# Optimization experiments

Measured on AMD Instinct MI355X. Metric: run time of the kernel, lower is better.

Reference implementation:

```python
import jax, jax.numpy as jnp
import numpy as np

D_MODEL = 768
NUM_HEADS = 12
D_K = D_MODEL // NUM_HEADS


def setup_inputs() -> dict:
    key = jax.random.key(0)
    ks = jax.random.split(key, 9)
    B, N, C = 32, 577, D_MODEL
    s = 1.0 / np.sqrt(C)
    x = jax.random.normal(ks[0], (B, N, C), dtype=jnp.float32)
    Wq = jax.random.normal(ks[1], (C, C), dtype=jnp.float32) * s
    bq = jnp.zeros((C,), dtype=jnp.float32)
    Wk = jax.random.normal(ks[2], (C, C), dtype=jnp.float32) * s
    bk = jnp.zeros((C,), dtype=jnp.float32)
    Wv = jax.random.normal(ks[3], (C, C), dtype=jnp.float32) * s
    bv = jnp.zeros((C,), dtype=jnp.float32)
    Wo = jax.random.normal(ks[4], (C, C), dtype=jnp.float32) * s
    bo = jnp.zeros((C,), dtype=jnp.float32)
    return {"x": x, "Wq": Wq, "bq": bq, "Wk": Wk, "bk": bk,
            "Wv": Wv, "bv": bv, "Wo": Wo, "bo": bo}


def reference(x, Wq, bq, Wk, bk, Wv, bv, Wo, bo):
    B, N, C = x.shape
    H, dk = NUM_HEADS, D_K
    # Linear projections (torch Linear: x @ W.T + b)
    q = (x @ Wq.T + bq).reshape(B, N, H, dk).transpose(0, 2, 1, 3)  # [B,H,N,dk]
    k = (x @ Wk.T + bk).reshape(B, N, H, dk).transpose(0, 2, 1, 3)
    v = (x @ Wv.T + bv).reshape(B, N, H, dk).transpose(0, 2, 1, 3)
    scale = 1.0 / jnp.sqrt(jnp.asarray(dk, dtype=x.dtype))
    scores = jnp.einsum('bhnd,bhmd->bhnm', q, k) * scale  # [B,H,N,N]
    attn = jax.nn.softmax(scores, axis=-1)
    out = jnp.einsum('bhnm,bhmd->bhnd', attn, v)  # [B,H,N,dk]
    out = out.transpose(0, 2, 1, 3).reshape(B, N, C)
    return out @ Wo.T + bo
```

## Files before the change

kernel.cpp:

```cpp
#include <hip/hip_runtime.h>
#include <cstdint>
#include <cstddef>

typedef float  f32x4   __attribute__((ext_vector_type(4)));
typedef __bf16 bf16x8  __attribute__((ext_vector_type(8)));
typedef short  short8  __attribute__((ext_vector_type(8)));
typedef short  short4v __attribute__((ext_vector_type(4)));
typedef float  float4v __attribute__((ext_vector_type(4)));

#define DEVI __device__ __forceinline__

constexpr int Bb = 32, Nn = 577, Cc = 768, Hh = 12, DK = 64;
constexpr int Mm   = Bb * Nn;
constexpr int NQKV = 3 * Cc;
constexpr int NKPAD = 640;
constexpr int NT = 10;
#define QSCALE 0.1803368926f

DEVI short f2bf(float f) {
  __bf16 h = (__bf16)f;
  short s;
  __builtin_memcpy(&s, &h, 2);
  return s;
}

DEVI void gload16(const short* g, short* l) {
  __builtin_amdgcn_global_load_lds(
      (const __attribute__((address_space(1))) void*)g,
      (__attribute__((address_space(3))) void*)l, 16, 0, 0);
}

DEVI f32x4 mfma16(bf16x8 a, bf16x8 b, f32x4 c) {
  return __builtin_amdgcn_mfma_f32_16x16x32_bf16(a, b, c, 0, 0, 0);
}

DEVI void remap_grouped(int bid, int nbm, int nbn, int GM, int& bm, int& bn) {
  const int nwg = nbm * nbn;
  const int xcd = bid & 7, j = bid >> 3;
  const int q = nwg >> 3, r = nwg & 7;
  int wg = (xcd < r ? xcd * (q + 1) : r * (q + 1) + (xcd - r) * q) + j;
  const int per = GM * nbn;
  int grp = wg / per;
  int first = grp * GM;
  int sz = min(GM, nbm - first);
  int rem = wg - grp * per;
  bm = first + rem % sz;
  bn = rem / sz;
}


__global__ void k_cvt(const float* __restrict__ in, short* __restrict__ out, int n4) {
  int i = blockIdx.x * 256 + threadIdx.x;
  if (i >= n4) return;
  float4v v = *(const float4v*)(in + (size_t)i * 4);
  short4v o;
#pragma unroll
  for (int j = 0; j < 4; ++j) o[j] = f2bf(v[j]);
  *(short4v*)(out + (size_t)i * 4) = o;
}

__global__ void k_cvt_wqkv(const float* __restrict__ Wq, const float* __restrict__ Wk,
                           const float* __restrict__ Wv, short* __restrict__ out) {
  int i = blockIdx.x * 256 + threadIdx.x;
  int e = i * 4;
  if (e >= NQKV * Cc) return;
  const int WSZ = Cc * Cc;
  const float* src;
  if (e < WSZ)          src = Wq + e;
  else if (e < 2 * WSZ) src = Wk + (e - WSZ);
  else                  src = Wv + (e - 2 * WSZ);
  float4v v = *(const float4v*)src;
  short4v o;
#pragma unroll
  for (int j = 0; j < 4; ++j) o[j] = f2bf(v[j]);
  *(short4v*)(out + (size_t)e) = o;
}


#define WAITV(N) asm volatile("s_waitcnt vmcnt(" #N ")" ::: "memory")

#define PHASE(DKH, MH, STAGE_STMT, WAIT_STMT)                              \
  {                                                                        \
    const short* Ab_ = Al + (DKH) * 8192;                                  \
    const short* Bb_ = Bl + (DKH) * 8192;                                  \
    bf16x8 af_[4];                                                         \
    _Pragma("unroll")                                                      \
    for (int m_ = 0; m_ < 4; ++m_)                                         \
      af_[m_] = *(const bf16x8*)(Ab_ + offA[(MH) * 4 + m_]);               \
    if ((MH) == 0) {                                                       \
      _Pragma("unroll")                                                    \
      for (int n_ = 0; n_ < 4; ++n_)                                       \
        bfr[n_] = *(const bf16x8*)(Bb_ + offB[n_]);                        \
    }                                                                      \
    STAGE_STMT;                                                            \
    WAIT_STMT;                                                             \
    __builtin_amdgcn_s_barrier();                                          \
    __builtin_amdgcn_s_setprio(1);                                         \
    _Pragma("unroll")                                                      \
    for (int m_ = 0; m_ < 4; ++m_)                                         \
      _Pragma("unroll")                                                    \
      for (int n_ = 0; n_ < 4; ++n_)                                       \
        acc[(MH) * 4 + m_][n_] = mfma16(af_[m_], bfr[n_], acc[(MH) * 4 + m_][n_]); \
    __builtin_amdgcn_s_setprio(0);                                         \
    __builtin_amdgcn_s_barrier();                                          \
  }

DEVI void gemm256_core(const short* __restrict__ A, const short* __restrict__ Bm,
                       int arows, int bm, int bn,
                       short* Al, short* Bl, f32x4 acc[8][4]) {
  const int tid = threadIdx.x;
  const int lane = tid & 63, w = tid >> 6;
  const int wm = w >> 2, wn = w & 3;
  const int qi = lane & 15, g = lane >> 4;

#pragma unroll
  for (int m = 0; m < 8; ++m)
#pragma unroll
    for (int n = 0; n < 4; ++n) acc[m][n] = (f32x4)0.0f;

  const int r0 = tid >> 2, gq = tid & 3;
  const int gs0 = (gq ^ ((r0 + (r0 >> 2)) & 3)) * 8;
  int ga0 = bm * 256 + r0;       if (ga0 > arows - 1) ga0 = arows - 1;
  int ga1 = bm * 256 + 128 + r0; if (ga1 > arows - 1) ga1 = arows - 1;
  const short* pA0 = A  + (size_t)ga0 * Cc + gs0;
  const short* pA1 = A  + (size_t)ga1 * Cc + gs0;
  const short* pB0 = Bm + (size_t)(bn * 256 + r0) * Cc + gs0;
  const short* pB1 = Bm + (size_t)(bn * 256 + 128 + r0) * Cc + gs0;

  auto stA = [&](int dkh, int coff) {
    short* d = Al + dkh * 8192 + w * 512;
    gload16(pA0 + coff, d);
    gload16(pA1 + coff, d + 4096);
  };
  auto stB = [&](int dkh, int coff) {
    short* d = Bl + dkh * 8192 + w * 512;
    gload16(pB0 + coff, d);
    gload16(pB1 + coff, d + 4096);
  };

  int offA[8], offB[4];
#pragma unroll
  for (int m = 0; m < 8; ++m) {
    int r = wm * 128 + m * 16 + qi;
    offA[m] = r * 32 + ((g ^ ((r + (r >> 2)) & 3)) * 8);
  }
#pragma unroll
  for (int n = 0; n < 4; ++n) {
    int r = wn * 64 + n * 16 + qi;
    offB[n] = r * 32 + ((g ^ ((r + (r >> 2)) & 3)) * 8);
  }
  bf16x8 bfr[4];

  stA(0, 0);  stB(0, 0);
  stA(1, 32); stB(1, 32);
  stA(2, 64); stB(2, 64);
  WAITV(4);
  __builtin_amdgcn_s_barrier();

#pragma unroll 1
  for (int i = 0; i < 5; ++i) {
    const int ko = i * 128;
    PHASE(0, 0, stA(3, ko + 96),  (void)0);
    PHASE(0, 1, stB(3, ko + 96),  WAITV(8));
    PHASE(1, 0, stA(0, ko + 128), (void)0);
    PHASE(1, 1, stB(0, ko + 128), WAITV(8));
    PHASE(2, 0, stA(1, ko + 160), (void)0);
    PHASE(2, 1, stB(1, ko + 160), WAITV(8));
    PHASE(3, 0, stA(2, ko + 192), (void)0);
    PHASE(3, 1, stB(2, ko + 192), WAITV(8));
  }
  PHASE(0, 0, stA(3, 736), (void)0);
  PHASE(0, 1, stB(3, 736), WAITV(8));
  PHASE(1, 0, (void)0, (void)0);
  PHASE(1, 1, (void)0, WAITV(4));
  PHASE(2, 0, (void)0, (void)0);
  PHASE(2, 1, (void)0, WAITV(0));
  PHASE(3, 0, (void)0, (void)0);
  PHASE(3, 1, (void)0, (void)0);
}

__global__ __launch_bounds__(512) void k_gemm_qkv(
    const short* __restrict__ A, const short* __restrict__ Bm,
    const float* __restrict__ bq, const float* __restrict__ bk, const float* __restrict__ bv,
    short* __restrict__ qv, short* __restrict__ kv, short* __restrict__ vv) {
  __shared__ short Al[4 * 8192];
  __shared__ short Bl[4 * 8192];
  int bm, bn;
  remap_grouped((int)blockIdx.x, (Mm + 255) / 256, NQKV / 256, 4, bm, bn);
  f32x4 acc[8][4];
  gemm256_core(A, Bm, Mm, bm, bn, Al, Bl, acc);

  const int lane = threadIdx.x & 63, w = threadIdx.x >> 6;
  const int wm = w >> 2, wn = w & 3;
  const int qi = lane & 15, g = lane >> 4;
  const int cb = bn * 256 + wn * 64;
  const int proj = cb / Cc;
  const int within = cb - proj * Cc;
  const float* bias = proj == 0 ? bq : proj == 1 ? bk : bv;
  short* dst = proj == 0 ? qv : proj == 1 ? kv : vv;
  const float sc = proj == 0 ? QSCALE : 1.0f;
  const int hh = within >> 6;
  float bvv[4];
#pragma unroll
  for (int n = 0; n < 4; ++n) bvv[n] = bias[within + n * 16 + qi];
#pragma unroll
  for (int m = 0; m < 8; ++m)
#pragma unroll
    for (int r = 0; r < 4; ++r) {
      int row = bm * 256 + wm * 128 + m * 16 + g * 4 + r;
      if (row < Mm) {
        int b = row / Nn;
        int nn = row - b * Nn;
        size_t base = ((size_t)(b * Hh + hh) * Nn + nn) * DK;
#pragma unroll
        for (int n = 0; n < 4; ++n)
          dst[base + n * 16 + qi] = f2bf((acc[m][n][r] + bvv[n]) * sc);
      }
    }
}

__global__ __launch_bounds__(512) void k_gemm_out(
    const short* __restrict__ A, const short* __restrict__ Bm,
    const float* __restrict__ bo, float* __restrict__ out) {
  __shared__ short Al[4 * 8192];
  __shared__ short Bl[4 * 8192];
  int bm, bn;
  remap_grouped((int)blockIdx.x, (Mm + 255) / 256, Cc / 256, 8, bm, bn);
  f32x4 acc[8][4];
  gemm256_core(A, Bm, Mm, bm, bn, Al, Bl, acc);

  const int lane = threadIdx.x & 63, w = threadIdx.x >> 6;
  const int wm = w >> 2, wn = w & 3;
  const int qi = lane & 15, g = lane >> 4;
  const int cb = bn * 256 + wn * 64;
  float bvv[4];
#pragma unroll
  for (int n = 0; n < 4; ++n) bvv[n] = bo[cb + n * 16 + qi];
#pragma unroll
  for (int m = 0; m < 8; ++m)
#pragma unroll
    for (int r = 0; r < 4; ++r) {
      int row = bm * 256 + wm * 128 + m * 16 + g * 4 + r;
      if (row < Mm) {
#pragma unroll
        for (int n = 0; n < 4; ++n)
          out[(size_t)row * Cc + cb + n * 16 + qi] = acc[m][n][r] + bvv[n];
      }
    }
}

__global__ __launch_bounds__(256) void k_transpose_v(const short* __restrict__ v,
                                                     short* __restrict__ vt) {
  __shared__ short t[64 * 72];
  const int bid = blockIdx.x;
  const int ch = bid % NT, bh = bid / NT;
  const int tid = threadIdx.x;
  const short* vb = v + (size_t)bh * Nn * DK;
#pragma unroll
  for (int i = 0; i < 2; ++i) {
    int gi = i * 256 + tid;
    int r = gi >> 3, c = gi & 7;
    int n = ch * 64 + r;
    short8 val;
#pragma unroll
    for (int j = 0; j < 8; ++j) val[j] = 0;
    if (n < Nn) val = *(const short8*)(vb + (size_t)n * DK + c * 8);
    *(short8*)(t + r * 72 + c * 8) = val;
  }
  __syncthreads();
  short* ob = vt + (size_t)bh * DK * NKPAD + ch * 64;
#pragma unroll
  for (int i = 0; i < 2; ++i) {
    int gi = i * 256 + tid;
    int d = gi >> 3, cg = gi & 7;
    short8 o;
#pragma unroll
    for (int j = 0; j < 8; ++j) o[j] = t[(cg * 8 + j) * 72 + d];
    *(short8*)(ob + (size_t)d * NKPAD + cg * 8) = o;
  }
}

__global__ __launch_bounds__(256) void k_attn(const short* __restrict__ q,
                                              const short* __restrict__ k,
                                              const short* __restrict__ vt,
                                              short* __restrict__ ao) {
  __shared__ short Ks[2][64 * 64];
  __shared__ short Vs[2][64 * 64];
  __shared__ short Ps[4][16 * 64];
  int bid = (int)blockIdx.x;
  bid = (bid & 7) * 480 + (bid >> 3);
  const int qt = bid % NT, bh = bid / NT;
  const int bb = bh / Hh, hh = bh - bb * Hh;
  const int tid = threadIdx.x, lane = tid & 63, w = tid >> 6;
  const int qi = lane & 15, g = lane >> 4;

  const short* qb  = q  + (size_t)bh * Nn * DK;
  const short* kb  = k  + (size_t)bh * Nn * DK;
  const short* vtb = vt + (size_t)bh * DK * NKPAD;

  const int qrow = qt * 64 + w * 16 + qi;
  const bf16x8 qf0 = *(const bf16x8*)(qb + (size_t)qrow * DK + g * 8);
  const bf16x8 qf1 = *(const bf16x8*)(qb + (size_t)qrow * DK + 32 + g * 8);

  const int r0 = tid >> 3, cc = tid & 7;
  const int cs0 = (cc ^ (r0 & 7)) * 8;
  const short* kg = kb + r0 * DK + cs0;
  const short* vg = vtb + (size_t)r0 * NKPAD + cs0;
  short* const Kd0 = &Ks[0][w * 512]; short* const Kd1 = &Ks[1][w * 512];
  short* const Vd0 = &Vs[0][w * 512]; short* const Vd1 = &Vs[1][w * 512];

  auto stage = [&](short* Kd, short* Vd) {
    gload16(kg, Kd);          gload16(kg + 2048,  Kd + 2048);
    gload16(vg, Vd);          gload16(vg + 20480, Vd + 2048);
    kg += 4096;               vg += 64;
  };

  const int swq = qi & 7;
  const short* const KF00 = &Ks[0][qi * 64 + ((g    ) ^ swq) * 8];
  const short* const KF01 = &Ks[0][qi * 64 + ((g + 4) ^ swq) * 8];
  const short* const KF10 = &Ks[1][qi * 64 + ((g    ) ^ swq) * 8];
  const short* const KF11 = &Ks[1][qi * 64 + ((g + 4) ^ swq) * 8];
  const short* const VF00 = &Vs[0][qi * 64 + ((g    ) ^ swq) * 8];
  const short* const VF01 = &Vs[0][qi * 64 + ((g + 4) ^ swq) * 8];
  const short* const VF10 = &Vs[1][qi * 64 + ((g    ) ^ swq) * 8];
  const short* const VF11 = &Vs[1][qi * 64 + ((g + 4) ^ swq) * 8];
  short* const PW0 = &Ps[w][qi * 64 + (((0  + g) ^ (swq << 1)) << 2)];
  short* const PW1 = &Ps[w][qi * 64 + (((4  + g) ^ (swq << 1)) << 2)];
  short* const PW2 = &Ps[w][qi * 64 + (((8  + g) ^ (swq << 1)) << 2)];
  short* const PW3 = &Ps[w][qi * 64 + (((12 + g) ^ (swq << 1)) << 2)];
  const short* const PR0 = &Ps[w][qi * 64 + ((g    ) ^ swq) * 8];
  const short* const PR1 = &Ps[w][qi * 64 + ((g + 4) ^ swq) * 8];

  f32x4 accd[4];
#pragma unroll
  for (int nd = 0; nd < 4; ++nd) accd[nd] = (f32x4)0.0f;
  float ls = 0.f;

  auto compute = [&](const short* Kf0, const short* Kf1,
                     const short* Vf0, const short* Vf1, bool last) {
    f32x4 s[4];
#pragma unroll
    for (int ni = 0; ni < 4; ++ni) s[ni] = (f32x4)0.0f;
#pragma unroll
    for (int ni = 0; ni < 4; ++ni)
      s[ni] = mfma16(*(const bf16x8*)(Kf0 + ni * 1024), qf0, s[ni]);
#pragma unroll
    for (int ni = 0; ni < 4; ++ni)
      s[ni] = mfma16(*(const bf16x8*)(Kf1 + ni * 1024), qf1, s[ni]);
    if (last) {
#pragma unroll
      for (int ni = 0; ni < 4; ++ni)
#pragma unroll
        for (int r = 0; r < 4; ++r)
          if (ni || r) s[ni][r] = -1e30f;
      if (g) s[0][0] = -1e30f;
    }
    float rs = 0.f;
    short4v pk0, pk1, pk2, pk3;
#pragma unroll
    for (int r = 0; r < 4; ++r) { float p = exp2f(s[0][r]); rs += p; pk0[r] = f2bf(p); }
#pragma unroll
    for (int r = 0; r < 4; ++r) { float p = exp2f(s[1][r]); rs += p; pk1[r] = f2bf(p); }
#pragma unroll
    for (int r = 0; r < 4; ++r) { float p = exp2f(s[2][r]); rs += p; pk2[r] = f2bf(p); }
#pragma unroll
    for (int r = 0; r < 4; ++r) { float p = exp2f(s[3][r]); rs += p; pk3[r] = f2bf(p); }
    *(short4v*)PW0 = pk0; *(short4v*)PW1 = pk1;
    *(short4v*)PW2 = pk2; *(short4v*)PW3 = pk3;
    rs += __shfl_xor(rs, 16);
    rs += __shfl_xor(rs, 32);
    ls += rs;
    bf16x8 pa0 = *(const bf16x8*)PR0;
    bf16x8 pa1 = *(const bf16x8*)PR1;
#pragma unroll
    for (int nd = 0; nd < 4; ++nd)
      accd[nd] = mfma16(pa0, *(const bf16x8*)(Vf0 + nd * 1024), accd[nd]);
#pragma unroll
    for (int nd = 0; nd < 4; ++nd)
      accd[nd] = mfma16(pa1, *(const bf16x8*)(Vf1 + nd * 1024), accd[nd]);
  };

  stage(Kd0, Vd0);
  __syncthreads();
#pragma unroll 1
  for (int t2 = 0; t2 < 5; ++t2) {
    stage(Kd1, Vd1);
    compute(KF00, KF01, VF00, VF01, false);
    __syncthreads();
    if (t2 < 4) {
      stage(Kd0, Vd0);
      compute(KF10, KF11, VF10, VF11, false);
      __syncthreads();
    }
  }
  compute(KF10, KF11, VF10, VF11, true);

  float ls4[4];
#pragma unroll
  for (int r = 0; r < 4; ++r) ls4[r] = __shfl(ls, (g << 2) + r);
#pragma unroll
  for (int r = 0; r < 4; ++r) {
    int qr = qt * 64 + w * 16 + (g << 2) + r;
    if (qr < Nn) {
      float inv = 1.0f / ls4[r];
      size_t base = ((size_t)(bb * Nn + qr)) * Cc + hh * DK;
#pragma unroll
      for (int nd = 0; nd < 4; ++nd)
        ao[base + nd * 16 + qi] = f2bf(accd[nd][r] * inv);
    }
  }
}


extern "C" void kernel_launch(void* const* d_in, const int* in_sizes, int n_in,
                              void* d_out, int out_size, void* d_ws, size_t ws_size,
                              hipStream_t stream) {
  const float* x  = (const float*)d_in[0];
  const float* Wq = (const float*)d_in[1];
  const float* bq = (const float*)d_in[2];
  const float* Wk = (const float*)d_in[3];
  const float* bk = (const float*)d_in[4];
  const float* Wv = (const float*)d_in[5];
  const float* bv = (const float*)d_in[6];
  const float* Wo = (const float*)d_in[7];
  const float* bo = (const float*)d_in[8];
  float* out = (float*)d_out;

  char* ws = (char*)d_ws;
  size_t off = 0;
  auto alloc = [&](size_t bytes) {
    char* p = ws + off;
    off += (bytes + 255) & ~(size_t)255;
    return p;
  };
  short* xb   = (short*)alloc((size_t)Mm * Cc * 2);
  short* wqkv = (short*)alloc((size_t)NQKV * Cc * 2);
  short* wob  = (short*)alloc((size_t)Cc * Cc * 2);
  short* qb   = (short*)alloc((size_t)Bb * Hh * Nn * DK * 2);
  short* kb   = (short*)alloc((size_t)Bb * Hh * Nn * DK * 2);
  short* vb   = (short*)alloc((size_t)Bb * Hh * Nn * DK * 2);
  short* vtb  = (short*)alloc((size_t)Bb * Hh * DK * NKPAD * 2);
  short* aob  = xb;

  k_cvt<<<(Mm * Cc / 4 + 255) / 256, 256, 0, stream>>>(x, xb, Mm * Cc / 4);
  k_cvt_wqkv<<<(NQKV * Cc / 4 + 255) / 256, 256, 0, stream>>>(Wq, Wk, Wv, wqkv);
  k_cvt<<<(Cc * Cc / 4 + 255) / 256, 256, 0, stream>>>(Wo, wob, Cc * Cc / 4);

  const int nbm = (Mm + 255) / 256;
  k_gemm_qkv<<<nbm * (NQKV / 256), 512, 0, stream>>>(xb, wqkv, bq, bk, bv, qb, kb, vb);

  k_transpose_v<<<Bb * Hh * NT, 256, 0, stream>>>(vb, vtb);

  k_attn<<<Bb * Hh * NT, 256, 0, stream>>>(qb, kb, vtb, aob);

  k_gemm_out<<<nbm * (Cc / 256), 512, 0, stream>>>(aob, wob, bo, out);
}
```

Baseline: 223.7 us.

## Fuse fp32-to-bf16 input conversion into QKV GEMM and process two query tiles per attention block

The QKV GEMM now reads fp32 x directly, converting to bf16 in registers and writing to LDS, which removes the separate conversion kernel and its extra round trip through global memory. Independently, the attention kernel handles two 64-row query tiles per block, reusing each staged K/V tile for both and halving the number of blocks. The fused path adds register pressure and reads twice the bytes per A element. Doubling work per attention block reduces the grid size and may lower occupancy or latency hiding.

```diff
diff --git a/kernel.cpp b/kernel.cpp
--- a/kernel.cpp
+++ b/kernel.cpp
@@ -75,7 +75,6 @@
   for (int j = 0; j < 4; ++j) o[j] = f2bf(v[j]);
   *(short4v*)(out + (size_t)e) = o;
 }
-
 
 #define WAITV(N) asm volatile("s_waitcnt vmcnt(" #N ")" ::: "memory")
 
@@ -179,8 +178,132 @@
   PHASE(3, 1, (void)0, (void)0);
 }
 
+DEVI void gemm256_fusedA(const float* __restrict__ X, const short* __restrict__ Bm,
+                         int bm, int bn, short* Al, short* Bl, f32x4 acc[8][4]) {
+  const int tid = threadIdx.x;
+  const int lane = tid & 63, w = tid >> 6;
+  const int wm = w >> 2, wn = w & 3;
+  const int qi = lane & 15, g = lane >> 4;
+
+#pragma unroll
+  for (int m = 0; m < 8; ++m)
+#pragma unroll
+    for (int n = 0; n < 4; ++n) acc[m][n] = (f32x4)0.0f;
+
+  const int r0 = tid >> 2, gq = tid & 3;
+  const int gs0 = (gq ^ ((r0 + (r0 >> 2)) & 3)) * 8;
+  int ga0 = bm * 256 + r0;       if (ga0 > Mm - 1) ga0 = Mm - 1;
+  int ga1 = bm * 256 + 128 + r0; if (ga1 > Mm - 1) ga1 = Mm - 1;
+  const float* xa0 = X + (size_t)ga0 * Cc + gs0;
+  const float* xa1 = X + (size_t)ga1 * Cc + gs0;
+  const short* pB0 = Bm + (size_t)(bn * 256 + r0) * Cc + gs0;
+  const short* pB1 = Bm + (size_t)(bn * 256 + 128 + r0) * Cc + gs0;
+
+  float4v ra0[4], ra1[4];
+  auto Is0 = [&](int sl) {
+    int co = sl * 32;
+    ra0[0] = *(const float4v*)(xa0 + co);     ra0[1] = *(const float4v*)(xa0 + co + 4);
+    ra0[2] = *(const float4v*)(xa1 + co);     ra0[3] = *(const float4v*)(xa1 + co + 4);
+  };
+  auto Is1 = [&](int sl) {
+    int co = sl * 32;
+    ra1[0] = *(const float4v*)(xa0 + co);     ra1[1] = *(const float4v*)(xa0 + co + 4);
+    ra1[2] = *(const float4v*)(xa1 + co);     ra1[3] = *(const float4v*)(xa1 + co + 4);
+  };
+  auto Wr0 = [&](int dkh) {
+    short* d = Al + dkh * 8192 + w * 512 + lane * 8;
+    bf16x8 lo, hi;
+#pragma unroll
+    for (int t = 0; t < 4; ++t) {
+      lo[t] = (__bf16)ra0[0][t]; lo[t + 4] = (__bf16)ra0[1][t];
+      hi[t] = (__bf16)ra0[2][t]; hi[t + 4] = (__bf16)ra0[3][t];
+    }
+    *(bf16x8*)d = lo; *(bf16x8*)(d + 4096) = hi;
+  };
+  auto Wr1 = [&](int dkh) {
+    short* d = Al + dkh * 8192 + w * 512 + lane * 8;
+    bf16x8 lo, hi;
+#pragma unroll
+    for (int t = 0; t < 4; ++t) {
+      lo[t] = (__bf16)ra1[0][t]; lo[t + 4] = (__bf16)ra1[1][t];
+      hi[t] = (__bf16)ra1[2][t]; hi[t + 4] = (__bf16)ra1[3][t];
+    }
+    *(bf16x8*)d = lo; *(bf16x8*)(d + 4096) = hi;
+  };
+  auto stB = [&](int dkh, int coff) {
+    short* d = Bl + dkh * 8192 + w * 512;
+    gload16(pB0 + coff, d);
+    gload16(pB1 + coff, d + 4096);
+  };
+
+  int offA[8], offB[4];
+#pragma unroll
+  for (int m = 0; m < 8; ++m) {
+    int r = wm * 128 + m * 16 + qi;
+    offA[m] = r * 32 + ((g ^ ((r + (r >> 2)) & 3)) * 8);
+  }
+#pragma unroll
+  for (int n = 0; n < 4; ++n) {
+    int r = wn * 64 + n * 16 + qi;
+    offB[n] = r * 32 + ((g ^ ((r + (r >> 2)) & 3)) * 8);
+  }
+  bf16x8 bfr[4];
+
+  Is1(0); Is0(1);
+  Wr1(0); Is1(2);
+  Wr0(1); Is0(3);
+  Wr1(2);
+  stB(0, 0); stB(1, 32); stB(2, 64);
+  Is1(4);
+  WAITV(8);
+  __builtin_amdgcn_s_barrier();
+
+#pragma unroll
+  for (int j = 0; j < 24; ++j) {
+    const int dkh = j & 3;
+    const short* Ab = Al + dkh * 8192;
+    const short* Bb = Bl + dkh * 8192;
+    {
+      bf16x8 af[4];
+#pragma unroll
+      for (int m = 0; m < 4; ++m) af[m] = *(const bf16x8*)(Ab + offA[m]);
+#pragma unroll
+      for (int n = 0; n < 4; ++n) bfr[n] = *(const bf16x8*)(Bb + offB[n]);
+      if (j + 3 < 24) { if ((j & 1) == 0) Wr0((j + 3) & 3); else Wr1((j + 3) & 3); }
+      if (j + 5 < 24) { if ((j & 1) == 0) Is0(j + 5);       else Is1(j + 5); }
+      __builtin_amdgcn_s_barrier();
+      __builtin_amdgcn_s_setprio(1);
+#pragma unroll
+      for (int m = 0; m < 4; ++m)
+#pragma unroll
+        for (int n = 0; n < 4; ++n) acc[m][n] = mfma16(af[m], bfr[n], acc[m][n]);
+      __builtin_amdgcn_s_setprio(0);
+      __builtin_amdgcn_s_barrier();
+    }
+    {
+      bf16x8 af[4];
+#pragma unroll
+      for (int m = 0; m < 4; ++m) af[m] = *(const bf16x8*)(Ab + offA[4 + m]);
+      if (j + 3 < 24) stB((j + 3) & 3, (j + 3) * 32);
+      if (j <= 18)      WAITV(12);
+      else if (j == 19) WAITV(8);
+      else if (j == 20) WAITV(4);
+      else if (j == 21) WAITV(2);
+      else if (j == 22) WAITV(0);
+      __builtin_amdgcn_s_barrier();
+      __builtin_amdgcn_s_setprio(1);
+#pragma unroll
+      for (int m = 0; m < 4; ++m)
+#pragma unroll
+        for (int n = 0; n < 4; ++n) acc[4 + m][n] = mfma16(af[m], bfr[n], acc[4 + m][n]);
+      __builtin_amdgcn_s_setprio(0);
+      __builtin_amdgcn_s_barrier();
+    }
+  }
+}
+
 __global__ __launch_bounds__(512) void k_gemm_qkv(
-    const short* __restrict__ A, const short* __restrict__ Bm,
+    const float* __restrict__ X, const short* __restrict__ Bm,
     const float* __restrict__ bq, const float* __restrict__ bk, const float* __restrict__ bv,
     short* __restrict__ qv, short* __restrict__ kv, short* __restrict__ vv) {
   __shared__ short Al[4 * 8192];
@@ -188,7 +311,7 @@
   int bm, bn;
   remap_grouped((int)blockIdx.x, (Mm + 255) / 256, NQKV / 256, 4, bm, bn);
   f32x4 acc[8][4];
-  gemm256_core(A, Bm, Mm, bm, bn, Al, Bl, acc);
+  gemm256_fusedA(X, Bm, bm, bn, Al, Bl, acc);
 
   const int lane = threadIdx.x & 63, w = threadIdx.x >> 6;
   const int wm = w >> 2, wn = w & 3;
@@ -288,8 +411,9 @@
   __shared__ short Vs[2][64 * 64];
   __shared__ short Ps[4][16 * 64];
   int bid = (int)blockIdx.x;
-  bid = (bid & 7) * 480 + (bid >> 3);
-  const int qt = bid % NT, bh = bid / NT;
+  bid = (bid & 7) * 240 + (bid >> 3);
+  const int qtp = bid % 5, bh = bid / 5;
+  const int qt0 = qtp * 2;
   const int bb = bh / Hh, hh = bh - bb * Hh;
   const int tid = threadIdx.x, lane = tid & 63, w = tid >> 6;
   const int qi = lane & 15, g = lane >> 4;
@@ -298,9 +422,11 @@
   const short* kb  = k  + (size_t)bh * Nn * DK;
   const short* vtb = vt + (size_t)bh * DK * NKPAD;
 
-  const int qrow = qt * 64 + w * 16 + qi;
-  const bf16x8 qf0 = *(const bf16x8*)(qb + (size_t)qrow * DK + g * 8);
-  const bf16x8 qf1 = *(const bf16x8*)(qb + (size_t)qrow * DK + 32 + g * 8);
+  const int qrow = qt0 * 64 + w * 16 + qi;
+  const bf16x8 qf0a = *(const bf16x8*)(qb + (size_t)qrow * DK + g * 8);
+  const bf16x8 qf1a = *(const bf16x8*)(qb + (size_t)qrow * DK + 32 + g * 8);
+  const bf16x8 qf0b = *(const bf16x8*)(qb + (size_t)(qrow + 64) * DK + g * 8);
+  const bf16x8 qf1b = *(const bf16x8*)(qb + (size_t)(qrow + 64) * DK + 32 + g * 8);
 
   const int r0 = tid >> 3, cc = tid & 7;
   const int cs0 = (cc ^ (r0 & 7)) * 8;
@@ -331,13 +457,14 @@
   const short* const PR0 = &Ps[w][qi * 64 + ((g    ) ^ swq) * 8];
   const short* const PR1 = &Ps[w][qi * 64 + ((g + 4) ^ swq) * 8];
 
-  f32x4 accd[4];
-#pragma unroll
-  for (int nd = 0; nd < 4; ++nd) accd[nd] = (f32x4)0.0f;
-  float ls = 0.f;
-
-  auto compute = [&](const short* Kf0, const short* Kf1,
-                     const short* Vf0, const short* Vf1, bool last) {
+  f32x4 accA[4], accB[4];
+#pragma unroll
+  for (int nd = 0; nd < 4; ++nd) { accA[nd] = (f32x4)0.0f; accB[nd] = (f32x4)0.0f; }
+  float lsA = 0.f, lsB = 0.f;
+
+  auto computeT = [&](const bf16x8& qf0, const bf16x8& qf1, f32x4* accd, float& ls,
+                      const short* Kf0, const short* Kf1,
+                      const short* Vf0, const short* Vf1, bool last) {
     f32x4 s[4];
 #pragma unroll
     for (int ni = 0; ni < 4; ++ni) s[ni] = (f32x4)0.0f;
@@ -385,30 +512,37 @@
 #pragma unroll 1
   for (int t2 = 0; t2 < 5; ++t2) {
     stage(Kd1, Vd1);
-    compute(KF00, KF01, VF00, VF01, false);
+    computeT(qf0a, qf1a, accA, lsA, KF00, KF01, VF00, VF01, false);
+    computeT(qf0b, qf1b, accB, lsB, KF00, KF01, VF00, VF01, false);
     __syncthreads();
     if (t2 < 4) {
       stage(Kd0, Vd0);
-      compute(KF10, KF11, VF10, VF11, false);
+      computeT(qf0a, qf1a, accA, lsA, KF10, KF11, VF10, VF11, false);
+      computeT(qf0b, qf1b, accB, lsB, KF10, KF11, VF10, VF11, false);
       __syncthreads();
     }
   }
-  compute(KF10, KF11, VF10, VF11, true);
-
-  float ls4[4];
-#pragma unroll
-  for (int r = 0; r < 4; ++r) ls4[r] = __shfl(ls, (g << 2) + r);
-#pragma unroll
-  for (int r = 0; r < 4; ++r) {
-    int qr = qt * 64 + w * 16 + (g << 2) + r;
-    if (qr < Nn) {
-      float inv = 1.0f / ls4[r];
-      size_t base = ((size_t)(bb * Nn + qr)) * Cc + hh * DK;
-#pragma unroll
-      for (int nd = 0; nd < 4; ++nd)
-        ao[base + nd * 16 + qi] = f2bf(accd[nd][r] * inv);
-    }
-  }
+  computeT(qf0a, qf1a, accA, lsA, KF10, KF11, VF10, VF11, true);
+  computeT(qf0b, qf1b, accB, lsB, KF10, KF11, VF10, VF11, true);
+
+  auto epi = [&](f32x4* accd, float ls, int qt) {
+    float ls4[4];
+#pragma unroll
+    for (int r = 0; r < 4; ++r) ls4[r] = __shfl(ls, (g << 2) + r);
+#pragma unroll
+    for (int r = 0; r < 4; ++r) {
+      int qr = qt * 64 + w * 16 + (g << 2) + r;
+      if (qr < Nn) {
+        float inv = 1.0f / ls4[r];
+        size_t base = ((size_t)(bb * Nn + qr)) * Cc + hh * DK;
+#pragma unroll
+        for (int nd = 0; nd < 4; ++nd)
+          ao[base + nd * 16 + qi] = f2bf(accd[nd][r] * inv);
+      }
+    }
+  };
+  epi(accA, lsA, qt0);
+  epi(accB, lsB, qt0 + 1);
 }
 
 
@@ -433,25 +567,23 @@
     off += (bytes + 255) & ~(size_t)255;
     return p;
   };
-  short* xb   = (short*)alloc((size_t)Mm * Cc * 2);
+  short* aob  = (short*)alloc((size_t)Mm * Cc * 2);
   short* wqkv = (short*)alloc((size_t)NQKV * Cc * 2);
   short* wob  = (short*)alloc((size_t)Cc * Cc * 2);
   short* qb   = (short*)alloc((size_t)Bb * Hh * Nn * DK * 2);
   short* kb   = (short*)alloc((size_t)Bb * Hh * Nn * DK * 2);
   short* vb   = (short*)alloc((size_t)Bb * Hh * Nn * DK * 2);
   short* vtb  = (short*)alloc((size_t)Bb * Hh * DK * NKPAD * 2);
-  short* aob  = xb;
-
-  k_cvt<<<(Mm * Cc / 4 + 255) / 256, 256, 0, stream>>>(x, xb, Mm * Cc / 4);
+
   k_cvt_wqkv<<<(NQKV * Cc / 4 + 255) / 256, 256, 0, stream>>>(Wq, Wk, Wv, wqkv);
   k_cvt<<<(Cc * Cc / 4 + 255) / 256, 256, 0, stream>>>(Wo, wob, Cc * Cc / 4);
 
   const int nbm = (Mm + 255) / 256;
-  k_gemm_qkv<<<nbm * (NQKV / 256), 512, 0, stream>>>(xb, wqkv, bq, bk, bv, qb, kb, vb);
+  k_gemm_qkv<<<nbm * (NQKV / 256), 512, 0, stream>>>(x, wqkv, bq, bk, bv, qb, kb, vb);
 
   k_transpose_v<<<Bb * Hh * NT, 256, 0, stream>>>(vb, vtb);
 
-  k_attn<<<Bb * Hh * NT, 256, 0, stream>>>(qb, kb, vtb, aob);
+  k_attn<<<Bb * Hh * 5, 256, 0, stream>>>(qb, kb, vtb, aob);
 
   k_gemm_out<<<nbm * (Cc / 256), 512, 0, stream>>>(aob, wob, bo, out);
 }
```

After: 232.5 us. 1.04x slower.

## Process two query tiles per attention block to reuse staged K/V tiles

Applied to the files above, without the earlier changes.

Each attention workgroup now handles two 64-row query tiles (128 rows) instead of one. Every K/V tile staged into shared memory, and every K/V fragment read from it, feeds both query tiles, which halves global K/V traffic and LDS fragment reads per query. The grid shrinks from 3840 to 1920 blocks, and each block holds twice the accumulators and a doubled P buffer. That raises register pressure and may lower occupancy.

```diff
diff --git a/kernel.cpp b/kernel.cpp
--- a/kernel.cpp
+++ b/kernel.cpp
@@ -75,7 +75,6 @@
   for (int j = 0; j < 4; ++j) o[j] = f2bf(v[j]);
   *(short4v*)(out + (size_t)e) = o;
 }
-
 
 #define WAITV(N) asm volatile("s_waitcnt vmcnt(" #N ")" ::: "memory")
 
@@ -286,10 +285,11 @@
                                               short* __restrict__ ao) {
   __shared__ short Ks[2][64 * 64];
   __shared__ short Vs[2][64 * 64];
-  __shared__ short Ps[4][16 * 64];
+  __shared__ short Ps[4][2][16 * 64];
   int bid = (int)blockIdx.x;
-  bid = (bid & 7) * 480 + (bid >> 3);
-  const int qt = bid % NT, bh = bid / NT;
+  bid = (bid & 7) * 240 + (bid >> 3);
+  const int qtp = bid % 5, bh = bid / 5;
+  const int qt0 = qtp * 2;
   const int bb = bh / Hh, hh = bh - bb * Hh;
   const int tid = threadIdx.x, lane = tid & 63, w = tid >> 6;
   const int qi = lane & 15, g = lane >> 4;
@@ -298,9 +298,11 @@
   const short* kb  = k  + (size_t)bh * Nn * DK;
   const short* vtb = vt + (size_t)bh * DK * NKPAD;
 
-  const int qrow = qt * 64 + w * 16 + qi;
-  const bf16x8 qf0 = *(const bf16x8*)(qb + (size_t)qrow * DK + g * 8);
-  const bf16x8 qf1 = *(const bf16x8*)(qb + (size_t)qrow * DK + 32 + g * 8);
+  const int qrow = qt0 * 64 + w * 16 + qi;
+  const bf16x8 qf0a = *(const bf16x8*)(qb + (size_t)qrow * DK + g * 8);
+  const bf16x8 qf1a = *(const bf16x8*)(qb + (size_t)qrow * DK + 32 + g * 8);
+  const bf16x8 qf0b = *(const bf16x8*)(qb + (size_t)(qrow + 64) * DK + g * 8);
+  const bf16x8 qf1b = *(const bf16x8*)(qb + (size_t)(qrow + 64) * DK + 32 + g * 8);
 
   const int r0 = tid >> 3, cc = tid & 7;
   const int cs0 = (cc ^ (r0 & 7)) * 8;
@@ -324,29 +326,21 @@
   const short* const VF01 = &Vs[0][qi * 64 + ((g + 4) ^ swq) * 8];
   const short* const VF10 = &Vs[1][qi * 64 + ((g    ) ^ swq) * 8];
   const short* const VF11 = &Vs[1][qi * 64 + ((g + 4) ^ swq) * 8];
-  short* const PW0 = &Ps[w][qi * 64 + (((0  + g) ^ (swq << 1)) << 2)];
-  short* const PW1 = &Ps[w][qi * 64 + (((4  + g) ^ (swq << 1)) << 2)];
-  short* const PW2 = &Ps[w][qi * 64 + (((8  + g) ^ (swq << 1)) << 2)];
-  short* const PW3 = &Ps[w][qi * 64 + (((12 + g) ^ (swq << 1)) << 2)];
-  const short* const PR0 = &Ps[w][qi * 64 + ((g    ) ^ swq) * 8];
-  const short* const PR1 = &Ps[w][qi * 64 + ((g + 4) ^ swq) * 8];
-
-  f32x4 accd[4];
-#pragma unroll
-  for (int nd = 0; nd < 4; ++nd) accd[nd] = (f32x4)0.0f;
-  float ls = 0.f;
-
-  auto compute = [&](const short* Kf0, const short* Kf1,
-                     const short* Vf0, const short* Vf1, bool last) {
-    f32x4 s[4];
-#pragma unroll
-    for (int ni = 0; ni < 4; ++ni) s[ni] = (f32x4)0.0f;
-#pragma unroll
-    for (int ni = 0; ni < 4; ++ni)
-      s[ni] = mfma16(*(const bf16x8*)(Kf0 + ni * 1024), qf0, s[ni]);
-#pragma unroll
-    for (int ni = 0; ni < 4; ++ni)
-      s[ni] = mfma16(*(const bf16x8*)(Kf1 + ni * 1024), qf1, s[ni]);
+  const int pwo0 = qi * 64 + (((0  + g) ^ (swq << 1)) << 2);
+  const int pwo1 = qi * 64 + (((4  + g) ^ (swq << 1)) << 2);
+  const int pwo2 = qi * 64 + (((8  + g) ^ (swq << 1)) << 2);
+  const int pwo3 = qi * 64 + (((12 + g) ^ (swq << 1)) << 2);
+  const int pro0 = qi * 64 + ((g    ) ^ swq) * 8;
+  const int pro1 = qi * 64 + ((g + 4) ^ swq) * 8;
+  short* const PA = &Ps[w][0][0];
+  short* const PB = &Ps[w][1][0];
+
+  f32x4 accA[4], accB[4];
+#pragma unroll
+  for (int nd = 0; nd < 4; ++nd) { accA[nd] = (f32x4)0.0f; accB[nd] = (f32x4)0.0f; }
+  float lsA = 0.f, lsB = 0.f;
+
+  auto smax = [&](f32x4* s, float& ls, short* P, bool last) {
     if (last) {
 #pragma unroll
       for (int ni = 0; ni < 4; ++ni)
@@ -365,19 +359,54 @@
     for (int r = 0; r < 4; ++r) { float p = exp2f(s[2][r]); rs += p; pk2[r] = f2bf(p); }
 #pragma unroll
     for (int r = 0; r < 4; ++r) { float p = exp2f(s[3][r]); rs += p; pk3[r] = f2bf(p); }
-    *(short4v*)PW0 = pk0; *(short4v*)PW1 = pk1;
-    *(short4v*)PW2 = pk2; *(short4v*)PW3 = pk3;
+    *(short4v*)(P + pwo0) = pk0; *(short4v*)(P + pwo1) = pk1;
+    *(short4v*)(P + pwo2) = pk2; *(short4v*)(P + pwo3) = pk3;
     rs += __shfl_xor(rs, 16);
     rs += __shfl_xor(rs, 32);
     ls += rs;
-    bf16x8 pa0 = *(const bf16x8*)PR0;
-    bf16x8 pa1 = *(const bf16x8*)PR1;
-#pragma unroll
-    for (int nd = 0; nd < 4; ++nd)
-      accd[nd] = mfma16(pa0, *(const bf16x8*)(Vf0 + nd * 1024), accd[nd]);
-#pragma unroll
-    for (int nd = 0; nd < 4; ++nd)
-      accd[nd] = mfma16(pa1, *(const bf16x8*)(Vf1 + nd * 1024), accd[nd]);
+  };
+
+  auto tilestep = [&](const short* Kf0, const short* Kf1,
+                      const short* Vf0, const short* Vf1, bool last) {
+    f32x4 sA[4], sB[4];
+#pragma unroll
+    for (int ni = 0; ni < 4; ++ni) { sA[ni] = (f32x4)0.0f; sB[ni] = (f32x4)0.0f; }
+    {
+      bf16x8 kf[4];
+#pragma unroll
+      for (int ni = 0; ni < 4; ++ni) kf[ni] = *(const bf16x8*)(Kf0 + ni * 1024);
+#pragma unroll
+      for (int ni = 0; ni < 4; ++ni) sA[ni] = mfma16(kf[ni], qf0a, sA[ni]);
+#pragma unroll
+      for (int ni = 0; ni < 4; ++ni) sB[ni] = mfma16(kf[ni], qf0b, sB[ni]);
+#pragma unroll
+      for (int ni = 0; ni < 4; ++ni) kf[ni] = *(const bf16x8*)(Kf1 + ni * 1024);
+#pragma unroll
+      for (int ni = 0; ni < 4; ++ni) sA[ni] = mfma16(kf[ni], qf1a, sA[ni]);
+#pragma unroll
+      for (int ni = 0; ni < 4; ++ni) sB[ni] = mfma16(kf[ni], qf1b, sB[ni]);
+    }
+    smax(sA, lsA, PA, last);
+    smax(sB, lsB, PB, last);
+    bf16x8 paA0 = *(const bf16x8*)(PA + pro0);
+    bf16x8 paA1 = *(const bf16x8*)(PA + pro1);
+    bf16x8 paB0 = *(const bf16x8*)(PB + pro0);
+    bf16x8 paB1 = *(const bf16x8*)(PB + pro1);
+    {
+      bf16x8 vf[4];
+#pragma unroll
+      for (int nd = 0; nd < 4; ++nd) vf[nd] = *(const bf16x8*)(Vf0 + nd * 1024);
+#pragma unroll
+      for (int nd = 0; nd < 4; ++nd) accA[nd] = mfma16(paA0, vf[nd], accA[nd]);
+#pragma unroll
+      for (int nd = 0; nd < 4; ++nd) accB[nd] = mfma16(paB0, vf[nd], accB[nd]);
+#pragma unroll
+      for (int nd = 0; nd < 4; ++nd) vf[nd] = *(const bf16x8*)(Vf1 + nd * 1024);
+#pragma unroll
+      for (int nd = 0; nd < 4; ++nd) accA[nd] = mfma16(paA1, vf[nd], accA[nd]);
+#pragma unroll
+      for (int nd = 0; nd < 4; ++nd) accB[nd] = mfma16(paB1, vf[nd], accB[nd]);
+    }
   };
 
   stage(Kd0, Vd0);
@@ -385,30 +414,34 @@
 #pragma unroll 1
   for (int t2 = 0; t2 < 5; ++t2) {
     stage(Kd1, Vd1);
-    compute(KF00, KF01, VF00, VF01, false);
+    tilestep(KF00, KF01, VF00, VF01, false);
     __syncthreads();
     if (t2 < 4) {
       stage(Kd0, Vd0);
-      compute(KF10, KF11, VF10, VF11, false);
+      tilestep(KF10, KF11, VF10, VF11, false);
       __syncthreads();
     }
   }
-  compute(KF10, KF11, VF10, VF11, true);
-
-  float ls4[4];
-#pragma unroll
-  for (int r = 0; r < 4; ++r) ls4[r] = __shfl(ls, (g << 2) + r);
-#pragma unroll
-  for (int r = 0; r < 4; ++r) {
-    int qr = qt * 64 + w * 16 + (g << 2) + r;
-    if (qr < Nn) {
-      float inv = 1.0f / ls4[r];
-      size_t base = ((size_t)(bb * Nn + qr)) * Cc + hh * DK;
-#pragma unroll
-      for (int nd = 0; nd < 4; ++nd)
-        ao[base + nd * 16 + qi] = f2bf(accd[nd][r] * inv);
-    }
-  }
+  tilestep(KF10, KF11, VF10, VF11, true);
+
+  auto epi = [&](f32x4* accd, float ls, int qt) {
+    float ls4[4];
+#pragma unroll
+    for (int r = 0; r < 4; ++r) ls4[r] = __shfl(ls, (g << 2) + r);
+#pragma unroll
+    for (int r = 0; r < 4; ++r) {
+      int qr = qt * 64 + w * 16 + (g << 2) + r;
+      if (qr < Nn) {
+        float inv = 1.0f / ls4[r];
+        size_t base = ((size_t)(bb * Nn + qr)) * Cc + hh * DK;
+#pragma unroll
+        for (int nd = 0; nd < 4; ++nd)
+          ao[base + nd * 16 + qi] = f2bf(accd[nd][r] * inv);
+      }
+    }
+  };
+  epi(accA, lsA, qt0);
+  epi(accB, lsB, qt0 + 1);
 }
 
 
@@ -451,7 +484,7 @@
 
   k_transpose_v<<<Bb * Hh * NT, 256, 0, stream>>>(vb, vtb);
 
-  k_attn<<<Bb * Hh * NT, 256, 0, stream>>>(qb, kb, vtb, aob);
+  k_attn<<<Bb * Hh * 5, 256, 0, stream>>>(qb, kb, vtb, aob);
 
   k_gemm_out<<<nbm * (Cc / 256), 512, 0, stream>>>(aob, wob, bo, out);
 }
```

New measurement: 223.9 us. No clear change (+0.1%).

## Process two query tiles per attention block and use BK=64 QKV GEMM pipeline

Applied to the files above, without the earlier changes.

The attention kernel now handles two 64-row query tiles per block, reusing each staged K/V tile for both and halving the grid. This cuts K/V global loads and LDS staging per query row. The QKV GEMM switches to a new core with 64-wide K slices in a double buffer and an interleaved staging schedule. The trade-off is more registers per attention thread (occupancy hint of 4) and fewer blocks to spread across CUs.

```diff
diff --git a/kernel.cpp b/kernel.cpp
--- a/kernel.cpp
+++ b/kernel.cpp
@@ -76,8 +76,106 @@
   *(short4v*)(out + (size_t)e) = o;
 }
 
-
 #define WAITV(N) asm volatile("s_waitcnt vmcnt(" #N ")" ::: "memory")
+
+#define GPH(BUF, KK, MH, STAGE, WAIT)                                      \
+  {                                                                        \
+    const short* Ab_ = Al + (BUF) * 16384;                                 \
+    const short* Bb_ = Bl + (BUF) * 16384;                                 \
+    bf16x8 af_[4];                                                         \
+    _Pragma("unroll")                                                      \
+    for (int m_ = 0; m_ < 4; ++m_)                                         \
+      af_[m_] = *(const bf16x8*)(Ab_ + (offA[(MH) * 4 + m_] ^ ((KK) * 32))); \
+    if ((MH) == 0) {                                                       \
+      _Pragma("unroll")                                                    \
+      for (int n_ = 0; n_ < 4; ++n_)                                       \
+        bfr[n_] = *(const bf16x8*)(Bb_ + (offB[n_] ^ ((KK) * 32)));        \
+    }                                                                      \
+    STAGE;                                                                 \
+    WAIT;                                                                  \
+    __builtin_amdgcn_s_barrier();                                          \
+    __builtin_amdgcn_s_setprio(1);                                         \
+    _Pragma("unroll")                                                      \
+    for (int m_ = 0; m_ < 4; ++m_)                                         \
+      _Pragma("unroll")                                                    \
+      for (int n_ = 0; n_ < 4; ++n_)                                       \
+        acc[(MH) * 4 + m_][n_] = mfma16(af_[m_], bfr[n_], acc[(MH) * 4 + m_][n_]); \
+    __builtin_amdgcn_s_setprio(0);                                         \
+    __builtin_amdgcn_s_barrier();                                          \
+  }
+
+DEVI void gemm256b(const short* __restrict__ A, const short* __restrict__ Bm,
+                   int arows, int bm, int bn,
+                   short* Al, short* Bl, f32x4 acc[8][4]) {
+  const int tid = threadIdx.x;
+  const int lane = tid & 63, w = tid >> 6;
+  const int wm = w >> 2, wn = w & 3;
+  const int qi = lane & 15, g = lane >> 4;
+
+#pragma unroll
+  for (int m = 0; m < 8; ++m)
+#pragma unroll
+    for (int n = 0; n < 4; ++n) acc[m][n] = (f32x4)0.0f;
+
+  const int rloc = tid >> 3, c8 = tid & 7;
+  const int gswz = (c8 ^ (rloc & 7)) * 8;
+  const short* pA[4];
+  const short* pB[4];
+#pragma unroll
+  for (int s = 0; s < 4; ++s) {
+    int ra = bm * 256 + s * 64 + rloc; if (ra > arows - 1) ra = arows - 1;
+    pA[s] = A  + (size_t)ra * Cc + gswz;
+    pB[s] = Bm + (size_t)(bn * 256 + s * 64 + rloc) * Cc + gswz;
+  }
+  auto stA = [&](int buf, int s, int co) {
+    gload16(pA[s] + co, Al + buf * 16384 + s * 4096 + tid * 8);
+  };
+  auto stB = [&](int buf, int s, int co) {
+    gload16(pB[s] + co, Bl + buf * 16384 + s * 4096 + tid * 8);
+  };
+
+  int offA[8], offB[4];
+#pragma unroll
+  for (int m = 0; m < 8; ++m) {
+    int r = wm * 128 + m * 16 + qi;
+    offA[m] = r * 64 + ((g ^ (r & 7)) * 8);
+  }
+#pragma unroll
+  for (int n = 0; n < 4; ++n) {
+    int r = wn * 64 + n * 16 + qi;
+    offB[n] = r * 64 + ((g ^ (r & 7)) * 8);
+  }
+  bf16x8 bfr[4];
+
+  stA(0, 0, 0); stA(0, 1, 0); stA(0, 2, 0); stA(0, 3, 0);
+  stB(0, 0, 0); stB(0, 1, 0); stB(0, 2, 0); stB(0, 3, 0);
+  stB(1, 0, 64); stB(1, 1, 64);
+  WAITV(2);
+  __builtin_amdgcn_s_barrier();
+
+#pragma unroll 1
+  for (int i = 0; i < 5; ++i) {
+    const int cb1  = 64 + 128 * i;
+    const int cb0n = cb1 + 64;
+    const int cb1n = cb1 + 128;
+    GPH(0, 0, 0, (stB(1, 2, cb1),  stB(1, 3, cb1)),  (void)0);
+    GPH(0, 0, 1, (stA(1, 0, cb1),  stA(1, 2, cb1)),  (void)0);
+    GPH(0, 1, 0, (stA(1, 1, cb1),  stA(1, 3, cb1)),  (void)0);
+    GPH(0, 1, 1, (stA(0, 0, cb0n), stA(0, 2, cb0n)), WAITV(4));
+    GPH(1, 0, 0, (stA(0, 1, cb0n), stA(0, 3, cb0n)), WAITV(4));
+    GPH(1, 0, 1, (stB(0, 0, cb0n), stB(0, 1, cb0n)), (void)0);
+    GPH(1, 1, 0, (stB(0, 2, cb0n), stB(0, 3, cb0n)), (void)0);
+    GPH(1, 1, 1, (stB(1, 0, cb1n), stB(1, 1, cb1n)), WAITV(2));
+  }
+  GPH(0, 0, 0, (stB(1, 2, 704), stB(1, 3, 704)), (void)0);
+  GPH(0, 0, 1, (stA(1, 0, 704), stA(1, 2, 704)), (void)0);
+  GPH(0, 1, 0, (stA(1, 1, 704), stA(1, 3, 704)), (void)0);
+  GPH(0, 1, 1, (void)0, WAITV(2));
+  GPH(1, 0, 0, (void)0, WAITV(0));
+  GPH(1, 0, 1, (void)0, (void)0);
+  GPH(1, 1, 0, (void)0, (void)0);
+  GPH(1, 1, 1, (void)0, (void)0);
+}
 
 #define PHASE(DKH, MH, STAGE_STMT, WAIT_STMT)                              \
   {                                                                        \
@@ -183,12 +281,12 @@
     const short* __restrict__ A, const short* __restrict__ Bm,
     const float* __restrict__ bq, const float* __restrict__ bk, const float* __restrict__ bv,
     short* __restrict__ qv, short* __restrict__ kv, short* __restrict__ vv) {
-  __shared__ short Al[4 * 8192];
-  __shared__ short Bl[4 * 8192];
+  __shared__ short Al[2 * 16384];
+  __shared__ short Bl[2 * 16384];
   int bm, bn;
   remap_grouped((int)blockIdx.x, (Mm + 255) / 256, NQKV / 256, 4, bm, bn);
   f32x4 acc[8][4];
-  gemm256_core(A, Bm, Mm, bm, bn, Al, Bl, acc);
+  gemm256b(A, Bm, Mm, bm, bn, Al, Bl, acc);
 
   const int lane = threadIdx.x & 63, w = threadIdx.x >> 6;
   const int wm = w >> 2, wn = w & 3;
@@ -280,16 +378,17 @@
   }
 }
 
-__global__ __launch_bounds__(256) void k_attn(const short* __restrict__ q,
-                                              const short* __restrict__ k,
-                                              const short* __restrict__ vt,
-                                              short* __restrict__ ao) {
+__global__ __launch_bounds__(256, 4) void k_attn(const short* __restrict__ q,
+                                                 const short* __restrict__ k,
+                                                 const short* __restrict__ vt,
+                                                 short* __restrict__ ao) {
   __shared__ short Ks[2][64 * 64];
   __shared__ short Vs[2][64 * 64];
   __shared__ short Ps[4][16 * 64];
   int bid = (int)blockIdx.x;
-  bid = (bid & 7) * 480 + (bid >> 3);
-  const int qt = bid % NT, bh = bid / NT;
+  bid = (bid & 7) * 240 + (bid >> 3);
+  const int qtp = bid % 5, bh = bid / 5;
+  const int qt0 = qtp * 2;
   const int bb = bh / Hh, hh = bh - bb * Hh;
   const int tid = threadIdx.x, lane = tid & 63, w = tid >> 6;
   const int qi = lane & 15, g = lane >> 4;
@@ -298,9 +397,11 @@
   const short* kb  = k  + (size_t)bh * Nn * DK;
   const short* vtb = vt + (size_t)bh * DK * NKPAD;
 
-  const int qrow = qt * 64 + w * 16 + qi;
-  const bf16x8 qf0 = *(const bf16x8*)(qb + (size_t)qrow * DK + g * 8);
-  const bf16x8 qf1 = *(const bf16x8*)(qb + (size_t)qrow * DK + 32 + g * 8);
+  const int qrow = qt0 * 64 + w * 16 + qi;
+  const bf16x8 qf0a = *(const bf16x8*)(qb + (size_t)qrow * DK + g * 8);
+  const bf16x8 qf1a = *(const bf16x8*)(qb + (size_t)qrow * DK + 32 + g * 8);
+  const bf16x8 qf0b = *(const bf16x8*)(qb + (size_t)(qrow + 64) * DK + g * 8);
+  const bf16x8 qf1b = *(const bf16x8*)(qb + (size_t)(qrow + 64) * DK + 32 + g * 8);
 
   const int r0 = tid >> 3, cc = tid & 7;
   const int cs0 = (cc ^ (r0 & 7)) * 8;
@@ -331,13 +432,14 @@
   const short* const PR0 = &Ps[w][qi * 64 + ((g    ) ^ swq) * 8];
   const short* const PR1 = &Ps[w][qi * 64 + ((g + 4) ^ swq) * 8];
 
-  f32x4 accd[4];
-#pragma unroll
-  for (int nd = 0; nd < 4; ++nd) accd[nd] = (f32x4)0.0f;
-  float ls = 0.f;
-
-  auto compute = [&](const short* Kf0, const short* Kf1,
-                     const short* Vf0, const short* Vf1, bool last) {
+  f32x4 accA[4], accB[4];
+#pragma unroll
+  for (int nd = 0; nd < 4; ++nd) { accA[nd] = (f32x4)0.0f; accB[nd] = (f32x4)0.0f; }
+  float lsA = 0.f, lsB = 0.f;
+
+  auto computeT = [&](const bf16x8& qf0, const bf16x8& qf1, f32x4* accd, float& ls,
+                      const short* Kf0, const short* Kf1,
+                      const short* Vf0, const short* Vf1, bool last) {
     f32x4 s[4];
 #pragma unroll
     for (int ni = 0; ni < 4; ++ni) s[ni] = (f32x4)0.0f;
@@ -385,30 +487,37 @@
 #pragma unroll 1
   for (int t2 = 0; t2 < 5; ++t2) {
     stage(Kd1, Vd1);
-    compute(KF00, KF01, VF00, VF01, false);
+    computeT(qf0a, qf1a, accA, lsA, KF00, KF01, VF00, VF01, false);
+    computeT(qf0b, qf1b, accB, lsB, KF00, KF01, VF00, VF01, false);
     __syncthreads();
     if (t2 < 4) {
       stage(Kd0, Vd0);
-      compute(KF10, KF11, VF10, VF11, false);
+      computeT(qf0a, qf1a, accA, lsA, KF10, KF11, VF10, VF11, false);
+      computeT(qf0b, qf1b, accB, lsB, KF10, KF11, VF10, VF11, false);
       __syncthreads();
     }
   }
-  compute(KF10, KF11, VF10, VF11, true);
-
-  float ls4[4];
-#pragma unroll
-  for (int r = 0; r < 4; ++r) ls4[r] = __shfl(ls, (g << 2) + r);
-#pragma unroll
-  for (int r = 0; r < 4; ++r) {
-    int qr = qt * 64 + w * 16 + (g << 2) + r;
-    if (qr < Nn) {
-      float inv = 1.0f / ls4[r];
-      size_t base = ((size_t)(bb * Nn + qr)) * Cc + hh * DK;
-#pragma unroll
-      for (int nd = 0; nd < 4; ++nd)
-        ao[base + nd * 16 + qi] = f2bf(accd[nd][r] * inv);
+  computeT(qf0a, qf1a, accA, lsA, KF10, KF11, VF10, VF11, true);
+  computeT(qf0b, qf1b, accB, lsB, KF10, KF11, VF10, VF11, true);
+
+  auto epi = [&](f32x4* accd, float ls, int qt) {
+    float ls4[4];
+#pragma unroll
+    for (int r = 0; r < 4; ++r) ls4[r] = __shfl(ls, (g << 2) + r);
+#pragma unroll
+    for (int r = 0; r < 4; ++r) {
+      int qr = qt * 64 + w * 16 + (g << 2) + r;
+      if (qr < Nn) {
+        float inv = 1.0f / ls4[r];
+        size_t base = ((size_t)(bb * Nn + qr)) * Cc + hh * DK;
+#pragma unroll
+        for (int nd = 0; nd < 4; ++nd)
+          ao[base + nd * 16 + qi] = f2bf(accd[nd][r] * inv);
+      }
     }
-  }
+  };
+  epi(accA, lsA, qt0);
+  epi(accB, lsB, qt0 + 1);
 }
 
 
@@ -451,7 +560,7 @@
 
   k_transpose_v<<<Bb * Hh * NT, 256, 0, stream>>>(vb, vtb);
 
-  k_attn<<<Bb * Hh * NT, 256, 0, stream>>>(qb, kb, vtb, aob);
+  k_attn<<<Bb * Hh * 5, 256, 0, stream>>>(qb, kb, vtb, aob);
 
   k_gemm_out<<<nbm * (Cc / 256), 512, 0, stream>>>(aob, wob, bo, out);
 }
```

After: 332.4 us. 48.6% more time.
